# Kernel optimization log

Measured on AMD Instinct MI355X. Metric: run time of the kernel, lower is better.

Reference implementation:

```python
import jax, jax.numpy as jnp
import numpy as np

EMBED_DIM = 512
NUM_HEADS = 16
WINDOW = 8
SHIFT = 4
NUM_PATCHES = 64
NEG_INF = -1e9


def _attention_mask():
    # group map over the full patch grid, as in calculate_attention_mask
    P, s, ws = NUM_PATCHES, SHIFT, WINDOW
    g = np.zeros((P, P), dtype=np.float32)
    g[:, -s:] = 1
    g[-s:, :] = 2
    g[-s:, -s:] = 3
    nw = P // ws
    # (h ws a, w ws b) -> (h*w, ws*ws)
    gw = g.reshape(nw, ws, nw, ws).transpose(0, 2, 1, 3).reshape(nw * nw, ws * ws)
    same = gw[:, None, :] == gw[:, :, None]  # column - row == 0 -> allowed
    return jnp.asarray(same)  # (nW, S, S) bool, True = keep


def setup_inputs() -> dict:
    key = jax.random.key(0)
    ks = jax.random.split(key, 5)
    B, P, C = 16, NUM_PATCHES, EMBED_DIM
    sd = 1.0 / np.sqrt(C)
    return {
        "x": jax.random.normal(ks[0], (B, P, P, C), dtype=jnp.float32),
        "w_qkv": jax.random.normal(ks[1], (3 * C, C), dtype=jnp.float32) * sd,
        "b_qkv": jax.random.normal(ks[2], (3 * C,), dtype=jnp.float32) * 0.02,
        "w_out": jax.random.normal(ks[3], (C, C), dtype=jnp.float32) * sd,
        "b_out": jax.random.normal(ks[4], (C,), dtype=jnp.float32) * 0.02,
    }


def reference(x, w_qkv, b_qkv, w_out, b_out):
    B, P, _, C = x.shape
    ws, H = WINDOW, NUM_HEADS
    d = C // H
    nw = P // ws
    S = ws * ws
    scale = d ** (-0.5)

    # shift (roll backwards)
    xs = jnp.roll(x, (-SHIFT, -SHIFT), axis=(1, 2))
    # window partition: (B, nw, ws, nw, ws, C) -> (B*nw*nw, S, C)
    xw = xs.reshape(B, nw, ws, nw, ws, C).transpose(0, 1, 3, 2, 4, 5)
    xw = xw.reshape(B * nw * nw, S, C)

    qkv = xw @ w_qkv.T + b_qkv  # (Bn, S, 3C)
    q, k, v = jnp.split(qkv, 3, axis=-1)
    # head partition: (Bn, S, H, d) -> (Bn, H, S, d)
    part = lambda t: t.reshape(-1, S, H, d).transpose(0, 2, 1, 3)
    q, k, v = part(q), part(k), part(v)

    scores = jnp.einsum('bhqd,bhkd->bhqk', q, k) * scale  # (Bn, H, S, S)

    mask = _attention_mask()  # (nW, S, S) bool
    scores = scores.reshape(B, nw * nw, H, S, S)
    scores = jnp.where(mask[None, :, None], scores, NEG_INF)
    attn = jax.nn.softmax(scores, axis=-1)  # dropout p=0 (inference)
    attn = attn.reshape(B * nw * nw, H, S, S)

    out = jnp.einsum('bhqk,bhkd->bhqd', attn, v)  # (Bn, H, S, d)
    out = out.transpose(0, 2, 1, 3).reshape(B * nw * nw, S, C)  # merge heads
    out = out @ w_out.T + b_out

    # window merge: (B*nw*nw, S, C) -> (B, P, P, C)
    out = out.reshape(B, nw, nw, ws, ws, C).transpose(0, 1, 3, 2, 4, 5)
    out = out.reshape(B, P, P, C)
    # roll forwards
    return jnp.roll(out, (SHIFT, SHIFT), axis=(1, 2))
```

## Files before the change

### kernel.cpp

```cpp
#include <hip/hip_runtime.h>


using f16   = _Float16;
using f16x8 = __attribute__((ext_vector_type(8))) _Float16;
using f16x4 = __attribute__((ext_vector_type(4))) _Float16;
using f32x4 = __attribute__((ext_vector_type(4))) float;

#define MFMA16(a, b, c) __builtin_amdgcn_mfma_f32_16x16x32_f16((a), (b), (c), 0, 0, 0)

static constexpr int QK_HALF = 65536 * 512;

__device__ __forceinline__ int tok2patch(int t) {
  int b = t >> 12, rem = t & 4095;
  int widx = rem >> 6, s = rem & 63;
  int pr = (((widx >> 3) << 3) + (s >> 3) + 4) & 63;
  int pc = (((widx & 7) << 3) + (s & 7) + 4) & 63;
  return ((b << 12) | (pr << 6) | pc) << 9;
}

__device__ __forceinline__ f16x8 cvt8(float4 a, float4 b) {
  f16x8 h = { (f16)a.x, (f16)a.y, (f16)a.z, (f16)a.w,
              (f16)b.x, (f16)b.y, (f16)b.z, (f16)b.w };
  return h;
}

__global__ __launch_bounds__(256) void k_qkv(const float* __restrict__ x,
                                             const float* __restrict__ wq,
                                             const float* __restrict__ bq,
                                             f16* __restrict__ qk,
                                             f16* __restrict__ vt) {
  __shared__ f16 As[128 * 32];
  __shared__ f16 Bs[128 * 32];
  __shared__ int rowoff[128];
  const int tid = threadIdx.x;
  const int bn = blockIdx.x;
  const int bm = blockIdx.y;
  if (tid < 128) rowoff[tid] = tok2patch(bm * 128 + tid);
  __syncthreads();
  const int lane = tid & 63, wave = tid >> 6;
  const int jlo = lane & 15, g = lane >> 4;
  const int wrow = (wave >> 1) * 64, wcol = (wave & 1) * 64;

  const int sr = tid >> 2, sc = tid & 3;
  const float* ax0 = x + rowoff[sr] + sc * 8;
  const float* ax1 = x + rowoff[sr + 64] + sc * 8;
  const float* bx0 = wq + (bn * 128 + sr) * 512 + sc * 8;
  const float* bx1 = bx0 + 64 * 512;
  f16* adst = (f16*)((char*)As + sr * 64 + 16 * (sc ^ ((sr >> 1) & 3)));
  f16* bdst = (f16*)((char*)Bs + sr * 64 + 16 * (sc ^ ((sr >> 1) & 3)));

  float4 r0, r1, r2, r3, r4, r5, r6, r7;
#define LOADT(K)                                                        \
  do {                                                                  \
    r0 = *(const float4*)(ax0 + (K)); r1 = *(const float4*)(ax0 + (K) + 4); \
    r2 = *(const float4*)(ax1 + (K)); r3 = *(const float4*)(ax1 + (K) + 4); \
    r4 = *(const float4*)(bx0 + (K)); r5 = *(const float4*)(bx0 + (K) + 4); \
    r6 = *(const float4*)(bx1 + (K)); r7 = *(const float4*)(bx1 + (K) + 4); \
  } while (0)

  f32x4 acc[4][4] = {};
  LOADT(0);
  for (int k0 = 0; k0 < 512; k0 += 32) {
    *(f16x8*)adst          = cvt8(r0, r1);
    *(f16x8*)(adst + 2048) = cvt8(r2, r3);
    *(f16x8*)bdst          = cvt8(r4, r5);
    *(f16x8*)(bdst + 2048) = cvt8(r6, r7);
    __syncthreads();
    if (k0 < 480) LOADT(k0 + 32);
    f16x8 af[4], bf[4];
#pragma unroll
    for (int mt = 0; mt < 4; ++mt) {
      int m = wrow + mt * 16 + jlo;
      af[mt] = *(const f16x8*)((const char*)As + m * 64 + 16 * (g ^ ((m >> 1) & 3)));
    }
#pragma unroll
    for (int nt = 0; nt < 4; ++nt) {
      int n = wcol + nt * 16 + jlo;
      bf[nt] = *(const f16x8*)((const char*)Bs + n * 64 + 16 * (g ^ ((n >> 1) & 3)));
    }
#pragma unroll
    for (int mt = 0; mt < 4; ++mt)
#pragma unroll
      for (int nt = 0; nt < 4; ++nt)
        acc[mt][nt] = MFMA16(af[mt], bf[nt], acc[mt][nt]);
    __syncthreads();
  }
#undef LOADT

#pragma unroll
  for (int nt = 0; nt < 4; ++nt) {
    const int colg = bn * 128 + wcol + nt * 16 + jlo;
    const float bias = bq[colg];
    if (colg < 1024) {
      const int base = (colg < 512) ? colg : (colg - 512 + QK_HALF);
#pragma unroll
      for (int mt = 0; mt < 4; ++mt) {
        const int t0 = bm * 128 + wrow + mt * 16 + g * 4;
#pragma unroll
        for (int r = 0; r < 4; ++r)
          qk[base + (t0 + r) * 512] = (f16)(acc[mt][nt][r] + bias);
      }
    } else {
      const int n = colg - 1024, h = n >> 5, d = n & 31;
#pragma unroll
      for (int mt = 0; mt < 4; ++mt) {
        const int t0 = bm * 128 + wrow + mt * 16 + g * 4;
        const int w = t0 >> 6, s0 = t0 & 63;
        f16x4 pk = { (f16)(acc[mt][nt][0] + bias), (f16)(acc[mt][nt][1] + bias),
                     (f16)(acc[mt][nt][2] + bias), (f16)(acc[mt][nt][3] + bias) };
        *(f16x4*)(vt + ((w * 16 + h) * 32 + d) * 64 + s0) = pk;
      }
    }
  }
}

__global__ __launch_bounds__(256) void k_attn(const f16* __restrict__ qk,
                                              const f16* __restrict__ vt,
                                              f16* __restrict__ ao) {
  __shared__ f16 P[4][64 * 72];
  const int w = blockIdx.x;
  const int widx = w & 63;
  const bool er = (widx >> 3) == 7;
  const bool ec = (widx & 7) == 7;
  const int tid = threadIdx.x;
  const int lane = tid & 63, wave = tid >> 6;
  const int jlo = lane & 15, g = lane >> 4;
  const int tb = w * 64;
  f16* Pw = P[wave];
  const float scale = 0.17677669529663687f;

#pragma unroll 1
  for (int hh = 0; hh < 4; ++hh) {
    const int h = wave * 4 + hh;
    f16x8 qa[4], kb[4];
#pragma unroll
    for (int mt = 0; mt < 4; ++mt)
      qa[mt] = *(const f16x8*)(qk + (tb + mt * 16 + jlo) * 512 + h * 32 + g * 8);
#pragma unroll
    for (int nt = 0; nt < 4; ++nt)
      kb[nt] = *(const f16x8*)(qk + QK_HALF + (tb + nt * 16 + jlo) * 512 + h * 32 + g * 8);
    f32x4 sc[4][4] = {};
#pragma unroll
    for (int mt = 0; mt < 4; ++mt)
#pragma unroll
      for (int nt = 0; nt < 4; ++nt)
        sc[mt][nt] = MFMA16(qa[mt], kb[nt], sc[mt][nt]);

    int gj[4];
#pragma unroll
    for (int nt = 0; nt < 4; ++nt) {
      int j = nt * 16 + jlo;
      gj[nt] = ((er && ((j >> 3) >= 4)) ? 2 : 0) | ((ec && ((j & 7) >= 4)) ? 1 : 0);
    }
    float rinv[4][4];
#pragma unroll
    for (int mt = 0; mt < 4; ++mt) {
#pragma unroll
      for (int r = 0; r < 4; ++r) {
        const int i = mt * 16 + g * 4 + r;
        const int gi = ((er && ((i >> 3) >= 4)) ? 2 : 0) | ((ec && ((i & 7) >= 4)) ? 1 : 0);
        float v0 = (gi == gj[0]) ? sc[mt][0][r] * scale : -1e9f;
        float v1 = (gi == gj[1]) ? sc[mt][1][r] * scale : -1e9f;
        float v2 = (gi == gj[2]) ? sc[mt][2][r] * scale : -1e9f;
        float v3 = (gi == gj[3]) ? sc[mt][3][r] * scale : -1e9f;
        float m = fmaxf(fmaxf(v0, v1), fmaxf(v2, v3));
        m = fmaxf(m, __shfl_xor(m, 1));
        m = fmaxf(m, __shfl_xor(m, 2));
        m = fmaxf(m, __shfl_xor(m, 4));
        m = fmaxf(m, __shfl_xor(m, 8));
        float p0 = __expf(v0 - m), p1 = __expf(v1 - m);
        float p2 = __expf(v2 - m), p3 = __expf(v3 - m);
        float s = p0 + p1 + p2 + p3;
        s += __shfl_xor(s, 1);
        s += __shfl_xor(s, 2);
        s += __shfl_xor(s, 4);
        s += __shfl_xor(s, 8);
        rinv[mt][r] = 1.0f / s;
        sc[mt][0][r] = p0; sc[mt][1][r] = p1; sc[mt][2][r] = p2; sc[mt][3][r] = p3;
      }
    }
#pragma unroll
    for (int mt = 0; mt < 4; ++mt)
#pragma unroll
      for (int nt = 0; nt < 4; ++nt)
#pragma unroll
        for (int r = 0; r < 4; ++r)
          Pw[(mt * 16 + g * 4 + r) * 72 + nt * 16 + jlo] = (f16)sc[mt][nt][r];
    asm volatile("s_waitcnt lgkmcnt(0)" ::: "memory");

    f32x4 o[4][2] = {};
#pragma unroll
    for (int ks = 0; ks < 2; ++ks) {
      f16x8 pa[4], vb[2];
#pragma unroll
      for (int mt = 0; mt < 4; ++mt)
        pa[mt] = *(const f16x8*)((const char*)Pw + (mt * 16 + jlo) * 144 + ks * 64 + g * 16);
#pragma unroll
      for (int nt = 0; nt < 2; ++nt)
        vb[nt] = *(const f16x8*)(vt + ((w * 16 + h) * 32 + nt * 16 + jlo) * 64 + ks * 32 + g * 8);
#pragma unroll
      for (int mt = 0; mt < 4; ++mt)
#pragma unroll
        for (int nt = 0; nt < 2; ++nt)
          o[mt][nt] = MFMA16(pa[mt], vb[nt], o[mt][nt]);
    }
#pragma unroll
    for (int mt = 0; mt < 4; ++mt)
#pragma unroll
      for (int nt = 0; nt < 2; ++nt)
#pragma unroll
        for (int r = 0; r < 4; ++r)
          ao[(tb + mt * 16 + g * 4 + r) * 512 + h * 32 + nt * 16 + jlo] =
              (f16)(o[mt][nt][r] * rinv[mt][r]);
  }
}

__global__ __launch_bounds__(256) void k_out(const f16* __restrict__ ao,
                                             const float* __restrict__ wo,
                                             const float* __restrict__ bo,
                                             float* __restrict__ out) {
  __shared__ f16 As[128 * 32];
  __shared__ f16 Bs[128 * 32];
  __shared__ int rowoff[128];
  const int tid = threadIdx.x;
  const int bn = blockIdx.x;
  const int bm = blockIdx.y;
  if (tid < 128) rowoff[tid] = tok2patch(bm * 128 + tid);
  __syncthreads();
  const int lane = tid & 63, wave = tid >> 6;
  const int jlo = lane & 15, g = lane >> 4;
  const int wrow = (wave >> 1) * 64, wcol = (wave & 1) * 64;

  const int sr = tid >> 2, sc = tid & 3;
  const f16* ax0 = ao + (bm * 128 + sr) * 512 + sc * 8;
  const f16* ax1 = ax0 + 64 * 512;
  const float* bx0 = wo + (bn * 128 + sr) * 512 + sc * 8;
  const float* bx1 = bx0 + 64 * 512;
  f16* adst = (f16*)((char*)As + sr * 64 + 16 * (sc ^ ((sr >> 1) & 3)));
  f16* bdst = (f16*)((char*)Bs + sr * 64 + 16 * (sc ^ ((sr >> 1) & 3)));

  f16x8 ha0, ha1;
  float4 r4, r5, r6, r7;
#define LOADT(K)                                                        \
  do {                                                                  \
    ha0 = *(const f16x8*)(ax0 + (K)); ha1 = *(const f16x8*)(ax1 + (K)); \
    r4 = *(const float4*)(bx0 + (K)); r5 = *(const float4*)(bx0 + (K) + 4); \
    r6 = *(const float4*)(bx1 + (K)); r7 = *(const float4*)(bx1 + (K) + 4); \
  } while (0)

  f32x4 acc[4][4] = {};
  LOADT(0);
  for (int k0 = 0; k0 < 512; k0 += 32) {
    *(f16x8*)adst          = ha0;
    *(f16x8*)(adst + 2048) = ha1;
    *(f16x8*)bdst          = cvt8(r4, r5);
    *(f16x8*)(bdst + 2048) = cvt8(r6, r7);
    __syncthreads();
    if (k0 < 480) LOADT(k0 + 32);
    f16x8 af[4], bf[4];
#pragma unroll
    for (int mt = 0; mt < 4; ++mt) {
      int m = wrow + mt * 16 + jlo;
      af[mt] = *(const f16x8*)((const char*)As + m * 64 + 16 * (g ^ ((m >> 1) & 3)));
    }
#pragma unroll
    for (int nt = 0; nt < 4; ++nt) {
      int n = wcol + nt * 16 + jlo;
      bf[nt] = *(const f16x8*)((const char*)Bs + n * 64 + 16 * (g ^ ((n >> 1) & 3)));
    }
#pragma unroll
    for (int mt = 0; mt < 4; ++mt)
#pragma unroll
      for (int nt = 0; nt < 4; ++nt)
        acc[mt][nt] = MFMA16(af[mt], bf[nt], acc[mt][nt]);
    __syncthreads();
  }
#undef LOADT

#pragma unroll
  for (int nt = 0; nt < 4; ++nt) {
    const int colg = bn * 128 + wcol + nt * 16 + jlo;
    const float bias = bo[colg];
#pragma unroll
    for (int mt = 0; mt < 4; ++mt) {
#pragma unroll
      for (int r = 0; r < 4; ++r)
        out[rowoff[wrow + mt * 16 + g * 4 + r] + colg] = acc[mt][nt][r] + bias;
    }
  }
}

extern "C" void kernel_launch(void* const* d_in, const int* in_sizes, int n_in,
                              void* d_out, int out_size, void* d_ws, size_t ws_size,
                              hipStream_t stream) {
  const float* x  = (const float*)d_in[0];
  const float* wq = (const float*)d_in[1];
  const float* bq = (const float*)d_in[2];
  const float* wo = (const float*)d_in[3];
  const float* bo = (const float*)d_in[4];
  float* out = (float*)d_out;

  f16* qk = (f16*)d_out;
  f16* vt = (f16*)d_ws;
  f16* ao = (f16*)((char*)d_ws + (64u << 20));

  k_qkv<<<dim3(12, 512), 256, 0, stream>>>(x, wq, bq, qk, vt);
  k_attn<<<dim3(1024), 256, 0, stream>>>(qk, vt, ao);
  k_out<<<dim3(4, 512), 256, 0, stream>>>(ao, wo, bo, out);
}
```

Before: 421.2 us.

## Pre-gather x to fp16, use direct global-to-LDS loads and BK=64 in GEMMs

```diff
diff --git a/kernel.cpp b/kernel.cpp
--- a/kernel.cpp
+++ b/kernel.cpp
@@ -9,6 +9,12 @@
 #define MFMA16(a, b, c) __builtin_amdgcn_mfma_f32_16x16x32_f16((a), (b), (c), 0, 0, 0)
 
 static constexpr int QK_HALF = 65536 * 512;
+
+typedef const __attribute__((address_space(1))) unsigned int* gp_t;
+typedef __attribute__((address_space(3))) unsigned int* sp_t;
+__device__ __forceinline__ void gl_lds16(const f16* g, f16* s) {
+  __builtin_amdgcn_global_load_lds((gp_t)g, (sp_t)s, 16, 0, 0);
+}
 
 __device__ __forceinline__ int tok2patch(int t) {
   int b = t >> 12, rem = t & 4095;
@@ -24,68 +30,84 @@
   return h;
 }
 
-__global__ __launch_bounds__(256) void k_qkv(const float* __restrict__ x,
+__global__ __launch_bounds__(256) void k_pre(const float* __restrict__ x,
+                                             f16* __restrict__ xg) {
+  const int t = blockIdx.x * 16 + (threadIdx.x >> 4);
+  const int i = threadIdx.x & 15;
+  const float4* src = (const float4*)(x + tok2patch(t));
+  f16x4* dst = (f16x4*)(xg + t * 512);
+#pragma unroll
+  for (int j = 0; j < 8; ++j) {
+    float4 v = src[i + j * 16];
+    f16x4 h = { (f16)v.x, (f16)v.y, (f16)v.z, (f16)v.w };
+    dst[i + j * 16] = h;
+  }
+}
+
+
+__global__ __launch_bounds__(256) void k_qkv(const f16* __restrict__ xg,
                                              const float* __restrict__ wq,
                                              const float* __restrict__ bq,
                                              f16* __restrict__ qk,
                                              f16* __restrict__ vt) {
-  __shared__ f16 As[128 * 32];
-  __shared__ f16 Bs[128 * 32];
-  __shared__ int rowoff[128];
+  __shared__ f16 As[128 * 64];
+  __shared__ f16 Bs[128 * 64];
+  const int bid = blockIdx.x;
+  const int wgid = (bid & 7) * 768 + (bid >> 3);
+  const int bm = wgid / 12, bn = wgid - bm * 12;
   const int tid = threadIdx.x;
-  const int bn = blockIdx.x;
-  const int bm = blockIdx.y;
-  if (tid < 128) rowoff[tid] = tok2patch(bm * 128 + tid);
-  __syncthreads();
   const int lane = tid & 63, wave = tid >> 6;
   const int jlo = lane & 15, g = lane >> 4;
   const int wrow = (wave >> 1) * 64, wcol = (wave & 1) * 64;
 
-  const int sr = tid >> 2, sc = tid & 3;
-  const float* ax0 = x + rowoff[sr] + sc * 8;
-  const float* ax1 = x + rowoff[sr + 64] + sc * 8;
-  const float* bx0 = wq + (bn * 128 + sr) * 512 + sc * 8;
-  const float* bx1 = bx0 + 64 * 512;
-  f16* adst = (f16*)((char*)As + sr * 64 + 16 * (sc ^ ((sr >> 1) & 3)));
-  f16* bdst = (f16*)((char*)Bs + sr * 64 + 16 * (sc ^ ((sr >> 1) & 3)));
-
-  float4 r0, r1, r2, r3, r4, r5, r6, r7;
-#define LOADT(K)                                                        \
-  do {                                                                  \
-    r0 = *(const float4*)(ax0 + (K)); r1 = *(const float4*)(ax0 + (K) + 4); \
-    r2 = *(const float4*)(ax1 + (K)); r3 = *(const float4*)(ax1 + (K) + 4); \
-    r4 = *(const float4*)(bx0 + (K)); r5 = *(const float4*)(bx0 + (K) + 4); \
-    r6 = *(const float4*)(bx1 + (K)); r7 = *(const float4*)(bx1 + (K) + 4); \
+  const int ar = wave * 32 + (lane >> 3);
+  const int aq = (lane & 7) ^ ((lane >> 3) & 7);
+  const f16* asrc = xg + (bm * 128 + ar) * 512 + aq * 8;
+  f16* aldsb = As + wave * 2048;
+
+  const int nl = tid & 127, h2 = tid >> 7;
+  const float* bsrc = wq + (bn * 128 + nl) * 512 + h2 * 32;
+
+  float4 rb[8];
+#define LOADB(K)                                                  \
+  do {                                                            \
+    _Pragma("unroll") for (int j = 0; j < 8; ++j)                 \
+        rb[j] = *(const float4*)(bsrc + (K) + j * 4);             \
   } while (0)
 
   f32x4 acc[4][4] = {};
-  LOADT(0);
-  for (int k0 = 0; k0 < 512; k0 += 32) {
-    *(f16x8*)adst          = cvt8(r0, r1);
-    *(f16x8*)(adst + 2048) = cvt8(r2, r3);
-    *(f16x8*)bdst          = cvt8(r4, r5);
-    *(f16x8*)(bdst + 2048) = cvt8(r6, r7);
+  LOADB(0);
+  for (int k0 = 0; k0 < 512; k0 += 64) {
+#pragma unroll
+    for (int i = 0; i < 4; ++i)
+      gl_lds16(asrc + k0 + i * 8 * 512, aldsb + i * 512);
+#pragma unroll
+    for (int q = 0; q < 4; ++q)
+      *(f16x8*)(Bs + nl * 64 + (((h2 * 4 + q) ^ (nl & 7)) * 8)) = cvt8(rb[2 * q], rb[2 * q + 1]);
     __syncthreads();
-    if (k0 < 480) LOADT(k0 + 32);
-    f16x8 af[4], bf[4];
-#pragma unroll
-    for (int mt = 0; mt < 4; ++mt) {
-      int m = wrow + mt * 16 + jlo;
-      af[mt] = *(const f16x8*)((const char*)As + m * 64 + 16 * (g ^ ((m >> 1) & 3)));
-    }
-#pragma unroll
-    for (int nt = 0; nt < 4; ++nt) {
-      int n = wcol + nt * 16 + jlo;
-      bf[nt] = *(const f16x8*)((const char*)Bs + n * 64 + 16 * (g ^ ((n >> 1) & 3)));
-    }
-#pragma unroll
-    for (int mt = 0; mt < 4; ++mt)
-#pragma unroll
-      for (int nt = 0; nt < 4; ++nt)
-        acc[mt][nt] = MFMA16(af[mt], bf[nt], acc[mt][nt]);
+    if (k0 < 448) LOADB(k0 + 64);
+#pragma unroll
+    for (int ks = 0; ks < 2; ++ks) {
+      f16x8 af[4], bf[4];
+#pragma unroll
+      for (int mt = 0; mt < 4; ++mt) {
+        int m = wrow + mt * 16 + jlo;
+        af[mt] = *(const f16x8*)(As + m * 64 + (((ks * 4 + g) ^ (m & 7)) * 8));
+      }
+#pragma unroll
+      for (int nt = 0; nt < 4; ++nt) {
+        int n = wcol + nt * 16 + jlo;
+        bf[nt] = *(const f16x8*)(Bs + n * 64 + (((ks * 4 + g) ^ (n & 7)) * 8));
+      }
+#pragma unroll
+      for (int mt = 0; mt < 4; ++mt)
+#pragma unroll
+        for (int nt = 0; nt < 4; ++nt)
+          acc[mt][nt] = MFMA16(af[mt], bf[nt], acc[mt][nt]);
+    }
     __syncthreads();
   }
-#undef LOADT
+#undef LOADB
 
 #pragma unroll
   for (int nt = 0; nt < 4; ++nt) {
@@ -219,63 +241,67 @@
                                              const float* __restrict__ wo,
                                              const float* __restrict__ bo,
                                              float* __restrict__ out) {
-  __shared__ f16 As[128 * 32];
-  __shared__ f16 Bs[128 * 32];
+  __shared__ f16 As[128 * 64];
+  __shared__ f16 Bs[128 * 64];
   __shared__ int rowoff[128];
+  const int bid = blockIdx.x;
+  const int wgid = (bid & 7) * 256 + (bid >> 3);
+  const int bm = wgid >> 2, bn = wgid & 3;
   const int tid = threadIdx.x;
-  const int bn = blockIdx.x;
-  const int bm = blockIdx.y;
   if (tid < 128) rowoff[tid] = tok2patch(bm * 128 + tid);
   __syncthreads();
   const int lane = tid & 63, wave = tid >> 6;
   const int jlo = lane & 15, g = lane >> 4;
   const int wrow = (wave >> 1) * 64, wcol = (wave & 1) * 64;
 
-  const int sr = tid >> 2, sc = tid & 3;
-  const f16* ax0 = ao + (bm * 128 + sr) * 512 + sc * 8;
-  const f16* ax1 = ax0 + 64 * 512;
-  const float* bx0 = wo + (bn * 128 + sr) * 512 + sc * 8;
-  const float* bx1 = bx0 + 64 * 512;
-  f16* adst = (f16*)((char*)As + sr * 64 + 16 * (sc ^ ((sr >> 1) & 3)));
-  f16* bdst = (f16*)((char*)Bs + sr * 64 + 16 * (sc ^ ((sr >> 1) & 3)));
-
-  f16x8 ha0, ha1;
-  float4 r4, r5, r6, r7;
-#define LOADT(K)                                                        \
-  do {                                                                  \
-    ha0 = *(const f16x8*)(ax0 + (K)); ha1 = *(const f16x8*)(ax1 + (K)); \
-    r4 = *(const float4*)(bx0 + (K)); r5 = *(const float4*)(bx0 + (K) + 4); \
-    r6 = *(const float4*)(bx1 + (K)); r7 = *(const float4*)(bx1 + (K) + 4); \
+  const int ar = wave * 32 + (lane >> 3);
+  const int aq = (lane & 7) ^ ((lane >> 3) & 7);
+  const f16* asrc = ao + (bm * 128 + ar) * 512 + aq * 8;
+  f16* aldsb = As + wave * 2048;
+
+  const int nl = tid & 127, h2 = tid >> 7;
+  const float* bsrc = wo + (bn * 128 + nl) * 512 + h2 * 32;
+
+  float4 rb[8];
+#define LOADB(K)                                                  \
+  do {                                                            \
+    _Pragma("unroll") for (int j = 0; j < 8; ++j)                 \
+        rb[j] = *(const float4*)(bsrc + (K) + j * 4);             \
   } while (0)
 
   f32x4 acc[4][4] = {};
-  LOADT(0);
-  for (int k0 = 0; k0 < 512; k0 += 32) {
-    *(f16x8*)adst          = ha0;
-    *(f16x8*)(adst + 2048) = ha1;
-    *(f16x8*)bdst          = cvt8(r4, r5);
-    *(f16x8*)(bdst + 2048) = cvt8(r6, r7);
+  LOADB(0);
+  for (int k0 = 0; k0 < 512; k0 += 64) {
+#pragma unroll
+    for (int i = 0; i < 4; ++i)
+      gl_lds16(asrc + k0 + i * 8 * 512, aldsb + i * 512);
+#pragma unroll
+    for (int q = 0; q < 4; ++q)
+      *(f16x8*)(Bs + nl * 64 + (((h2 * 4 + q) ^ (nl & 7)) * 8)) = cvt8(rb[2 * q], rb[2 * q + 1]);
     __syncthreads();
-    if (k0 < 480) LOADT(k0 + 32);
-    f16x8 af[4], bf[4];
-#pragma unroll
-    for (int mt = 0; mt < 4; ++mt) {
-      int m = wrow + mt * 16 + jlo;
-      af[mt] = *(const f16x8*)((const char*)As + m * 64 + 16 * (g ^ ((m >> 1) & 3)));
-    }
-#pragma unroll
-    for (int nt = 0; nt < 4; ++nt) {
-      int n = wcol + nt * 16 + jlo;
-      bf[nt] = *(const f16x8*)((const char*)Bs + n * 64 + 16 * (g ^ ((n >> 1) & 3)));
-    }
-#pragma unroll
-    for (int mt = 0; mt < 4; ++mt)
-#pragma unroll
-      for (int nt = 0; nt < 4; ++nt)
-        acc[mt][nt] = MFMA16(af[mt], bf[nt], acc[mt][nt]);
+    if (k0 < 448) LOADB(k0 + 64);
+#pragma unroll
+    for (int ks = 0; ks < 2; ++ks) {
+      f16x8 af[4], bf[4];
+#pragma unroll
+      for (int mt = 0; mt < 4; ++mt) {
+        int m = wrow + mt * 16 + jlo;
+        af[mt] = *(const f16x8*)(As + m * 64 + (((ks * 4 + g) ^ (m & 7)) * 8));
+      }
+#pragma unroll
+      for (int nt = 0; nt < 4; ++nt) {
+        int n = wcol + nt * 16 + jlo;
+        bf[nt] = *(const f16x8*)(Bs + n * 64 + (((ks * 4 + g) ^ (n & 7)) * 8));
+      }
+#pragma unroll
+      for (int mt = 0; mt < 4; ++mt)
+#pragma unroll
+        for (int nt = 0; nt < 4; ++nt)
+          acc[mt][nt] = MFMA16(af[mt], bf[nt], acc[mt][nt]);
+    }
     __syncthreads();
   }
-#undef LOADT
+#undef LOADB
 
 #pragma unroll
   for (int nt = 0; nt < 4; ++nt) {
@@ -301,10 +327,12 @@
   float* out = (float*)d_out;
 
   f16* qk = (f16*)d_out;
-  f16* vt = (f16*)d_ws;
-  f16* ao = (f16*)((char*)d_ws + (64u << 20));
-
-  k_qkv<<<dim3(12, 512), 256, 0, stream>>>(x, wq, bq, qk, vt);
+  f16* xg = (f16*)d_ws;
+  f16* vt = (f16*)((char*)d_ws + (64u << 20));
+  f16* ao = xg;
+
+  k_pre<<<dim3(4096), 256, 0, stream>>>(x, xg);
+  k_qkv<<<dim3(6144), 256, 0, stream>>>(xg, wq, bq, qk, vt);
   k_attn<<<dim3(1024), 256, 0, stream>>>(qk, vt, ao);
-  k_out<<<dim3(4, 512), 256, 0, stream>>>(ao, wo, bo, out);
-}
+  k_out<<<dim3(2048), 256, 0, stream>>>(ao, wo, bo, out);
+}
```

Result: slower. 476.1 us (+13.0%).
